# Kernel tuning notes

Hardware: AMD Instinct MI355X
Metric: run time of the kernel (lower is better)

## Reference

```python
import jax, jax.numpy as jnp
import numpy as np

NUM_BINS = 10
HIST_RANGE = 10.0
LN_EPS = 1e-5
NUM_SERVERS = 64
START_IDX = 2 + 2 + NUM_SERVERS  # = 68


def layer_norm(x, g, b):
    mu = jnp.mean(x, axis=-1, keepdims=True)
    var = jnp.mean(jnp.square(x - mu), axis=-1, keepdims=True)
    return (x - mu) * jax.lax.rsqrt(var + LN_EPS) * g + b


def batched_histogram(w):
    # w: [B, S]; replicates np.histogram(w_i, bins=10, range=(0,10)) per row,
    # then normalizes by (sum + 1e-8). Values outside [0,10] are excluded;
    # value == 10 falls in the last bin.
    idx = jnp.clip(jnp.floor(w * (NUM_BINS / HIST_RANGE)).astype(jnp.int32), 0, NUM_BINS - 1)
    mask = ((w >= 0.0) & (w <= HIST_RANGE)).astype(w.dtype)
    oh = jax.nn.one_hot(idx, NUM_BINS, dtype=w.dtype) * mask[..., None]  # [B,S,NB]
    hist = jnp.sum(oh, axis=1)  # [B,NB]
    return hist / (jnp.sum(hist, axis=-1, keepdims=True) + 1e-8)


def setup_inputs() -> dict:
    key = jax.random.key(0)
    ks = jax.random.split(key, 16)
    B, OBS, ACT, H, NB = 65536, 512, 64, 128, NUM_BINS
    COMB = (OBS - NUM_SERVERS) + 128 + 64  # 640

    def lin(k, fin, fout):
        bound = 1.0 / np.sqrt(fin)
        kw, kb = jax.random.split(k)
        return (jax.random.uniform(kw, (fin, fout), jnp.float32, -bound, bound),
                jax.random.uniform(kb, (fout,), jnp.float32, -bound, bound))

    obs = jax.random.uniform(ks[0], (B, OBS), jnp.float32, 0.0, 10.0)
    preference = jax.random.uniform(ks[1], (B, 2), jnp.float32)
    h_w1, h_b1 = lin(ks[2], NB, H)
    h_w2, h_b2 = lin(ks[3], H, H)
    p_w, p_b = lin(ks[4], 2, 64)
    s_w1, s_b1 = lin(ks[5], COMB, 256)
    s_w2, s_b2 = lin(ks[6], 256, 256)
    qd_w, qd_b = lin(ks[7], 256, ACT)
    qe_w, qe_b = lin(ks[8], 256, ACT)
    return {
        'obs': obs, 'preference': preference,
        'h_w1': h_w1, 'h_b1': h_b1,
        'h_ln1_g': jnp.ones((H,)), 'h_ln1_b': jnp.zeros((H,)),
        'h_w2': h_w2, 'h_b2': h_b2,
        'h_ln2_g': jnp.ones((H,)), 'h_ln2_b': jnp.zeros((H,)),
        'p_w': p_w, 'p_b': p_b,
        'p_ln_g': jnp.ones((64,)), 'p_ln_b': jnp.zeros((64,)),
        's_w1': s_w1, 's_b1': s_b1,
        's_ln1_g': jnp.ones((256,)), 's_ln1_b': jnp.zeros((256,)),
        's_w2': s_w2, 's_b2': s_b2,
        's_ln2_g': jnp.ones((256,)), 's_ln2_b': jnp.zeros((256,)),
        'qd_w': qd_w, 'qd_b': qd_b, 'qe_w': qe_w, 'qe_b': qe_b,
    }


def reference(obs, preference,
              h_w1, h_b1, h_ln1_g, h_ln1_b, h_w2, h_b2, h_ln2_g, h_ln2_b,
              p_w, p_b, p_ln_g, p_ln_b,
              s_w1, s_b1, s_ln1_g, s_ln1_b, s_w2, s_b2, s_ln2_g, s_ln2_b,
              qd_w, qd_b, qe_w, qe_b):
    server_workloads = obs[:, START_IDX:START_IDX + NUM_SERVERS]
    obs_wo = jnp.concatenate([obs[:, :START_IDX], obs[:, START_IDX + NUM_SERVERS:]], axis=-1)

    hist = batched_histogram(server_workloads)  # [B, 10]
    h = layer_norm(jax.nn.relu(hist @ h_w1 + h_b1), h_ln1_g, h_ln1_b)
    h = layer_norm(jax.nn.relu(h @ h_w2 + h_b2), h_ln2_g, h_ln2_b)  # [B,128]

    p = layer_norm(jax.nn.relu(preference @ p_w + p_b), p_ln_g, p_ln_b)  # [B,64]

    combined = jnp.concatenate([obs_wo, h, p], axis=-1)  # [B,640]
    s = layer_norm(jax.nn.relu(combined @ s_w1 + s_b1), s_ln1_g, s_ln1_b)
    s = layer_norm(jax.nn.relu(s @ s_w2 + s_b2), s_ln2_g, s_ln2_b)  # [B,256]

    q_delay = s @ qd_w + qd_b   # [B,A]
    q_energy = s @ qe_w + qe_b  # [B,A]
    return jnp.stack([q_delay, q_energy], axis=-1)  # [B,A,2]
```

## Files before the change

kernel.cpp:

```cpp
#include <hip/hip_runtime.h>

typedef __bf16 bf16x8 __attribute__((ext_vector_type(8)));
typedef __bf16 bf16x4 __attribute__((ext_vector_type(4)));
typedef float  f32x4  __attribute__((ext_vector_type(4)));

#define OFF_W1  0
#define OFF_W2  163840
#define OFF_WQ  229376
#define OFF_WH1 262144
#define OFF_WH2 266240
#define WS_ELEMS 282624

__global__ __launch_bounds__(256) void prep_kernel(
    const float* __restrict__ s_w1, const float* __restrict__ s_w2,
    const float* __restrict__ qd_w, const float* __restrict__ qe_w,
    const float* __restrict__ h_w1, const float* __restrict__ h_w2,
    __bf16* __restrict__ wsb)
{
  int idx = blockIdx.x * 256 + threadIdx.x;
  if (idx >= WS_ELEMS) return;
  float val = 0.f;
  if (idx < OFF_W2) {
    int t = idx;
    int j = t & 7, l = (t >> 3) & 63, rest = t >> 9;
    int nt = rest & 15, ks = rest >> 4;
    int k = ks * 32 + (l >> 4) * 8 + j, n = nt * 16 + (l & 15);
    val = s_w1[k * 256 + n];
  } else if (idx < OFF_WQ) {
    int t = idx - OFF_W2;
    int j = t & 7, l = (t >> 3) & 63, rest = t >> 9;
    int nt = rest & 15, ks = rest >> 4;
    int k = ks * 32 + (l >> 4) * 8 + j, n = nt * 16 + (l & 15);
    val = s_w2[k * 256 + n];
  } else if (idx < OFF_WH1) {
    int t = idx - OFF_WQ;
    int j = t & 7, l = (t >> 3) & 63, rest = t >> 9;
    int nt = rest & 7, ks = rest >> 3;
    int k = ks * 32 + (l >> 4) * 8 + j, n = nt * 16 + (l & 15);
    int a = n >> 1;
    val = (n & 1) ? qe_w[k * 64 + a] : qd_w[k * 64 + a];
  } else if (idx < OFF_WH2) {
    int t = idx - OFF_WH1;
    int j = t & 7, l = (t >> 3) & 63, rest = t >> 9;
    int nt = rest & 7;
    int k = (l >> 4) * 8 + j, n = nt * 16 + (l & 15);
    val = (k < 10) ? h_w1[k * 128 + n] : 0.f;
  } else {
    int t = idx - OFF_WH2;
    int j = t & 7, l = (t >> 3) & 63, rest = t >> 9;
    int nt = rest & 7, ks = rest >> 3;
    int k = ks * 32 + (l >> 4) * 8 + j, n = nt * 16 + (l & 15);
    val = h_w2[k * 128 + n];
  }
  wsb[idx] = (__bf16)val;
}

template<int KSTEPS, int NT_TOT, int NTW>
__device__ __forceinline__ void run_gemm(const __bf16* A, int astride,
    const bf16x8* __restrict__ Bsw, int wave, int lane, f32x4 acc[2][NTW])
{
  const int quad = lane >> 4, ln = lane & 15;
  const int ntb = wave * NTW;
  constexpr int PF = (KSTEPS >= 2) ? 2 : 1;
  bf16x8 bbuf[PF][NTW];
#pragma unroll
  for (int p = 0; p < PF; ++p)
#pragma unroll
    for (int i = 0; i < NTW; ++i)
      bbuf[p][i] = Bsw[(p * NT_TOT + ntb + i) * 64 + lane];
#pragma unroll
  for (int ks = 0; ks < KSTEPS; ++ks) {
    bf16x8 a[2];
#pragma unroll
    for (int mt = 0; mt < 2; ++mt)
      a[mt] = *(const bf16x8*)(A + (mt * 16 + ln) * astride + ks * 32 + quad * 8);
    bf16x8 bcur[NTW];
#pragma unroll
    for (int i = 0; i < NTW; ++i) bcur[i] = bbuf[ks % PF][i];
    if (ks + PF < KSTEPS) {
#pragma unroll
      for (int i = 0; i < NTW; ++i)
        bbuf[ks % PF][i] = Bsw[((ks + PF) * NT_TOT + ntb + i) * 64 + lane];
    }
#pragma unroll
    for (int mt = 0; mt < 2; ++mt)
#pragma unroll
      for (int i = 0; i < NTW; ++i)
        acc[mt][i] = __builtin_amdgcn_mfma_f32_16x16x32_bf16(a[mt], bcur[i], acc[mt][i], 0, 0, 0);
  }
}

template<int W, int NTW>
__device__ __forceinline__ void epilogue_ln(f32x4 acc[2][NTW],
    const float* __restrict__ bias, const float* __restrict__ g, const float* __restrict__ bb,
    __bf16* Adst, int dstride, int dstcol0,
    float* red_s, float* red_q, int wave, int lane)
{
  const int quad = lane >> 4, ln = lane & 15;
  float bv[NTW];
#pragma unroll
  for (int i = 0; i < NTW; ++i) bv[i] = bias[(wave * NTW + i) * 16 + ln];
#pragma unroll
  for (int mt = 0; mt < 2; ++mt) {
    float s[4] = {0, 0, 0, 0}, q[4] = {0, 0, 0, 0};
#pragma unroll
    for (int i = 0; i < NTW; ++i)
#pragma unroll
      for (int r = 0; r < 4; ++r) {
        float x = fmaxf(acc[mt][i][r] + bv[i], 0.f);
        s[r] += x; q[r] += x * x;
      }
#pragma unroll
    for (int m2 = 1; m2 < 16; m2 <<= 1)
#pragma unroll
      for (int r = 0; r < 4; ++r) {
        s[r] += __shfl_xor(s[r], m2, 64);
        q[r] += __shfl_xor(q[r], m2, 64);
      }
    if (ln == 0) {
#pragma unroll
      for (int r = 0; r < 4; ++r) {
        int m = mt * 16 + quad * 4 + r;
        red_s[wave * 32 + m] = s[r];
        red_q[wave * 32 + m] = q[r];
      }
    }
  }
  __syncthreads();
#pragma unroll
  for (int mt = 0; mt < 2; ++mt)
#pragma unroll
    for (int r = 0; r < 4; ++r) {
      int m = mt * 16 + quad * 4 + r;
      float tot = 0.f, totq = 0.f;
#pragma unroll
      for (int w2 = 0; w2 < 8; ++w2) { tot += red_s[w2 * 32 + m]; totq += red_q[w2 * 32 + m]; }
      float mu = tot / (float)W;
      float var = totq / (float)W - mu * mu;
      float rs = rsqrtf(var + 1e-5f);
#pragma unroll
      for (int i = 0; i < NTW; ++i) {
        int n = (wave * NTW + i) * 16 + ln;
        float x = fmaxf(acc[mt][i][r] + bv[i], 0.f);
        float o = (x - mu) * rs * g[n] + bb[n];
        Adst[m * dstride + dstcol0 + n] = (__bf16)o;
      }
    }
  __syncthreads();
}

__global__ __launch_bounds__(512)
__attribute__((amdgpu_waves_per_eu(4, 4)))
void critic_kernel(
    const float* __restrict__ obs, const float* __restrict__ pref,
    const float* __restrict__ h_b1, const float* __restrict__ h_g1, const float* __restrict__ h_bb1,
    const float* __restrict__ h_b2, const float* __restrict__ h_g2, const float* __restrict__ h_bb2,
    const float* __restrict__ p_w, const float* __restrict__ p_b,
    const float* __restrict__ p_g, const float* __restrict__ p_bb,
    const float* __restrict__ s_b1, const float* __restrict__ s_g1, const float* __restrict__ s_bb1,
    const float* __restrict__ s_b2, const float* __restrict__ s_g2, const float* __restrict__ s_bb2,
    const float* __restrict__ qd_b, const float* __restrict__ qe_b,
    const __bf16* __restrict__ wsb, float* __restrict__ out)
{
  __shared__ __align__(16) __bf16 A_comb[32 * 648];
  __shared__ __align__(16) __bf16 A_s[32 * 264];
  __shared__ __align__(16) __bf16 A_h[32 * 40];
  __shared__ float red_s[256];
  __shared__ float red_q[256];

  const int tid = threadIdx.x;
  const int wave = tid >> 6, lane = tid & 63;
  const int rowbase = blockIdx.x * 32;

  float pw0 = p_w[lane], pw1 = p_w[64 + lane], pb = p_b[lane];
  float pg = p_g[lane], pbb = p_bb[lane];
#pragma unroll
  for (int r = 0; r < 4; ++r) {
    int row = wave * 4 + r;
    int grow = rowbase + row;
    const float* orow = obs + (size_t)grow * 512;
    {
      int col = lane * 4;
      int src = (col < 68) ? col : col + 64;
      float4 v = *(const float4*)(orow + src);
      bf16x4 b4 = { (__bf16)v.x, (__bf16)v.y, (__bf16)v.z, (__bf16)v.w };
      *(bf16x4*)&A_comb[row * 648 + col] = b4;
    }
    if (lane < 48) {
      int col = 256 + lane * 4;
      float4 v = *(const float4*)(orow + col + 64);
      bf16x4 b4 = { (__bf16)v.x, (__bf16)v.y, (__bf16)v.z, (__bf16)v.w };
      *(bf16x4*)&A_comb[row * 648 + col] = b4;
    }
    float w = orow[68 + lane];
    int bi = (int)floorf(w);
    bi = bi < 0 ? 0 : (bi > 9 ? 9 : bi);
    bool valid = (w >= 0.f) && (w <= 10.f);
    float tot = 0.f, mine = 0.f;
#pragma unroll
    for (int b = 0; b < 10; ++b) {
      unsigned long long mk = __ballot(valid && (bi == b));
      float c = (float)__popcll(mk);
      tot += c;
      if (lane == b) mine = c;
    }
    float inv = 1.f / (tot + 1e-8f);
    if (lane < 32) A_h[row * 40 + lane] = (__bf16)((lane < 10) ? mine * inv : 0.f);
    float a0 = pref[grow * 2], a1 = pref[grow * 2 + 1];
    float v = fmaxf(fmaf(a0, pw0, fmaf(a1, pw1, pb)), 0.f);
    float s1 = v, s2 = v * v;
#pragma unroll
    for (int m2 = 1; m2 < 64; m2 <<= 1) {
      s1 += __shfl_xor(s1, m2, 64);
      s2 += __shfl_xor(s2, m2, 64);
    }
    float mu = s1 * (1.f / 64.f);
    float var = s2 * (1.f / 64.f) - mu * mu;
    float o = (v - mu) * rsqrtf(var + 1e-5f) * pg + pbb;
    A_comb[row * 648 + 576 + lane] = (__bf16)o;
  }
  __syncthreads();

  {
    f32x4 acc[2][1] = {};
    run_gemm<1, 8, 1>(A_h, 40, (const bf16x8*)(wsb + OFF_WH1), wave, lane, acc);
    epilogue_ln<128, 1>(acc, h_b1, h_g1, h_bb1, A_s, 264, 0, red_s, red_q, wave, lane);
  }
  {
    f32x4 acc[2][1] = {};
    run_gemm<4, 8, 1>(A_s, 264, (const bf16x8*)(wsb + OFF_WH2), wave, lane, acc);
    epilogue_ln<128, 1>(acc, h_b2, h_g2, h_bb2, A_comb, 648, 448, red_s, red_q, wave, lane);
  }
  {
    f32x4 acc[2][2] = {};
    run_gemm<20, 16, 2>(A_comb, 648, (const bf16x8*)(wsb + OFF_W1), wave, lane, acc);
    epilogue_ln<256, 2>(acc, s_b1, s_g1, s_bb1, A_s, 264, 0, red_s, red_q, wave, lane);
  }
  {
    f32x4 acc[2][2] = {};
    run_gemm<8, 16, 2>(A_s, 264, (const bf16x8*)(wsb + OFF_W2), wave, lane, acc);
    epilogue_ln<256, 2>(acc, s_b2, s_g2, s_bb2, A_s, 264, 0, red_s, red_q, wave, lane);
  }
  {
    f32x4 acc[2][1] = {};
    run_gemm<8, 8, 1>(A_s, 264, (const bf16x8*)(wsb + OFF_WQ), wave, lane, acc);
    const int quad = lane >> 4, ln = lane & 15;
    int n = wave * 16 + ln;
    float qb = (n & 1) ? qe_b[n >> 1] : qd_b[n >> 1];
#pragma unroll
    for (int mt = 0; mt < 2; ++mt)
#pragma unroll
      for (int r = 0; r < 4; ++r) {
        int m = mt * 16 + quad * 4 + r;
        out[(size_t)(rowbase + m) * 128 + n] = acc[mt][0][r] + qb;
      }
  }
}

extern "C" void kernel_launch(void* const* d_in, const int* in_sizes, int n_in,
                              void* d_out, int out_size, void* d_ws, size_t ws_size,
                              hipStream_t stream) {
  const float* obs    = (const float*)d_in[0];
  const float* pref   = (const float*)d_in[1];
  const float* h_w1   = (const float*)d_in[2];
  const float* h_b1   = (const float*)d_in[3];
  const float* h_g1   = (const float*)d_in[4];
  const float* h_bb1  = (const float*)d_in[5];
  const float* h_w2   = (const float*)d_in[6];
  const float* h_b2   = (const float*)d_in[7];
  const float* h_g2   = (const float*)d_in[8];
  const float* h_bb2  = (const float*)d_in[9];
  const float* p_w    = (const float*)d_in[10];
  const float* p_b    = (const float*)d_in[11];
  const float* p_g    = (const float*)d_in[12];
  const float* p_bb   = (const float*)d_in[13];
  const float* s_w1   = (const float*)d_in[14];
  const float* s_b1   = (const float*)d_in[15];
  const float* s_g1   = (const float*)d_in[16];
  const float* s_bb1  = (const float*)d_in[17];
  const float* s_w2   = (const float*)d_in[18];
  const float* s_b2   = (const float*)d_in[19];
  const float* s_g2   = (const float*)d_in[20];
  const float* s_bb2  = (const float*)d_in[21];
  const float* qd_w   = (const float*)d_in[22];
  const float* qd_b   = (const float*)d_in[23];
  const float* qe_w   = (const float*)d_in[24];
  const float* qe_b   = (const float*)d_in[25];

  __bf16* wsb = (__bf16*)d_ws;
  int B = in_sizes[0] / 512;
  int nblocks = B / 32;

  prep_kernel<<<(WS_ELEMS + 255) / 256, 256, 0, stream>>>(s_w1, s_w2, qd_w, qe_w, h_w1, h_w2, wsb);
  critic_kernel<<<nblocks, 512, 0, stream>>>(
      obs, pref, h_b1, h_g1, h_bb1, h_b2, h_g2, h_bb2,
      p_w, p_b, p_g, p_bb, s_b1, s_g1, s_bb1, s_b2, s_g2, s_bb2,
      qd_b, qe_b, (const __bf16*)wsb, (float*)d_out);
}
```

Before: 404.6 us.

## Split fused critic kernel into frontend and s-MLP kernels via bf16 global buffer

```diff
diff --git a/kernel.cpp b/kernel.cpp
--- a/kernel.cpp
+++ b/kernel.cpp
@@ -10,6 +10,7 @@
 #define OFF_WH1 262144
 #define OFF_WH2 266240
 #define WS_ELEMS 282624
+#define OFF_COMB 282624
 
 __global__ __launch_bounds__(256) void prep_kernel(
     const float* __restrict__ s_w1, const float* __restrict__ s_w2,
@@ -55,45 +56,43 @@
   wsb[idx] = (__bf16)val;
 }
 
-template<int KSTEPS, int NT_TOT, int NTW>
+template<int MT, int KSTEPS, int NT_TOT, int NTW>
 __device__ __forceinline__ void run_gemm(const __bf16* A, int astride,
-    const bf16x8* __restrict__ Bsw, int wave, int lane, f32x4 acc[2][NTW])
+    const bf16x8* __restrict__ Bsw, int wave, int lane, f32x4 acc[MT][NTW])
 {
   const int quad = lane >> 4, ln = lane & 15;
   const int ntb = wave * NTW;
-  constexpr int PF = (KSTEPS >= 2) ? 2 : 1;
-  bf16x8 bbuf[PF][NTW];
-#pragma unroll
-  for (int p = 0; p < PF; ++p)
-#pragma unroll
-    for (int i = 0; i < NTW; ++i)
-      bbuf[p][i] = Bsw[(p * NT_TOT + ntb + i) * 64 + lane];
+  bf16x8 bcur[NTW];
+#pragma unroll
+  for (int i = 0; i < NTW; ++i) bcur[i] = Bsw[(ntb + i) * 64 + lane];
 #pragma unroll
   for (int ks = 0; ks < KSTEPS; ++ks) {
-    bf16x8 a[2];
-#pragma unroll
-    for (int mt = 0; mt < 2; ++mt)
+    bf16x8 bnxt[NTW];
+    if (ks + 1 < KSTEPS) {
+#pragma unroll
+      for (int i = 0; i < NTW; ++i)
+        bnxt[i] = Bsw[((ks + 1) * NT_TOT + ntb + i) * 64 + lane];
+    }
+    bf16x8 a[MT];
+#pragma unroll
+    for (int mt = 0; mt < MT; ++mt)
       a[mt] = *(const bf16x8*)(A + (mt * 16 + ln) * astride + ks * 32 + quad * 8);
-    bf16x8 bcur[NTW];
-#pragma unroll
-    for (int i = 0; i < NTW; ++i) bcur[i] = bbuf[ks % PF][i];
-    if (ks + PF < KSTEPS) {
-#pragma unroll
-      for (int i = 0; i < NTW; ++i)
-        bbuf[ks % PF][i] = Bsw[((ks + PF) * NT_TOT + ntb + i) * 64 + lane];
-    }
-#pragma unroll
-    for (int mt = 0; mt < 2; ++mt)
+#pragma unroll
+    for (int mt = 0; mt < MT; ++mt)
 #pragma unroll
       for (int i = 0; i < NTW; ++i)
         acc[mt][i] = __builtin_amdgcn_mfma_f32_16x16x32_bf16(a[mt], bcur[i], acc[mt][i], 0, 0, 0);
-  }
-}
-
-template<int W, int NTW>
-__device__ __forceinline__ void epilogue_ln(f32x4 acc[2][NTW],
+    if (ks + 1 < KSTEPS) {
+#pragma unroll
+      for (int i = 0; i < NTW; ++i) bcur[i] = bnxt[i];
+    }
+  }
+}
+
+template<int MT, int W, int NTW, int NWAVES>
+__device__ __forceinline__ void epilogue_ln(f32x4 acc[MT][NTW],
     const float* __restrict__ bias, const float* __restrict__ g, const float* __restrict__ bb,
-    __bf16* Adst, int dstride, int dstcol0,
+    __bf16* dst, int dstride, int dstcol0,
     float* red_s, float* red_q, int wave, int lane)
 {
   const int quad = lane >> 4, ln = lane & 15;
@@ -101,7 +100,7 @@
 #pragma unroll
   for (int i = 0; i < NTW; ++i) bv[i] = bias[(wave * NTW + i) * 16 + ln];
 #pragma unroll
-  for (int mt = 0; mt < 2; ++mt) {
+  for (int mt = 0; mt < MT; ++mt) {
     float s[4] = {0, 0, 0, 0}, q[4] = {0, 0, 0, 0};
 #pragma unroll
     for (int i = 0; i < NTW; ++i)
@@ -121,20 +120,20 @@
 #pragma unroll
       for (int r = 0; r < 4; ++r) {
         int m = mt * 16 + quad * 4 + r;
-        red_s[wave * 32 + m] = s[r];
-        red_q[wave * 32 + m] = q[r];
+        red_s[wave * (MT * 16) + m] = s[r];
+        red_q[wave * (MT * 16) + m] = q[r];
       }
     }
   }
   __syncthreads();
 #pragma unroll
-  for (int mt = 0; mt < 2; ++mt)
+  for (int mt = 0; mt < MT; ++mt)
 #pragma unroll
     for (int r = 0; r < 4; ++r) {
       int m = mt * 16 + quad * 4 + r;
       float tot = 0.f, totq = 0.f;
 #pragma unroll
-      for (int w2 = 0; w2 < 8; ++w2) { tot += red_s[w2 * 32 + m]; totq += red_q[w2 * 32 + m]; }
+      for (int w2 = 0; w2 < NWAVES; ++w2) { tot += red_s[w2 * (MT * 16) + m]; totq += red_q[w2 * (MT * 16) + m]; }
       float mu = tot / (float)W;
       float var = totq / (float)W - mu * mu;
       float rs = rsqrtf(var + 1e-5f);
@@ -143,54 +142,49 @@
         int n = (wave * NTW + i) * 16 + ln;
         float x = fmaxf(acc[mt][i][r] + bv[i], 0.f);
         float o = (x - mu) * rs * g[n] + bb[n];
-        Adst[m * dstride + dstcol0 + n] = (__bf16)o;
+        dst[m * dstride + dstcol0 + n] = (__bf16)o;
       }
     }
   __syncthreads();
 }
 
-__global__ __launch_bounds__(512)
-__attribute__((amdgpu_waves_per_eu(4, 4)))
-void critic_kernel(
+__global__ __launch_bounds__(256) void frontend_kernel(
     const float* __restrict__ obs, const float* __restrict__ pref,
     const float* __restrict__ h_b1, const float* __restrict__ h_g1, const float* __restrict__ h_bb1,
     const float* __restrict__ h_b2, const float* __restrict__ h_g2, const float* __restrict__ h_bb2,
     const float* __restrict__ p_w, const float* __restrict__ p_b,
     const float* __restrict__ p_g, const float* __restrict__ p_bb,
-    const float* __restrict__ s_b1, const float* __restrict__ s_g1, const float* __restrict__ s_bb1,
-    const float* __restrict__ s_b2, const float* __restrict__ s_g2, const float* __restrict__ s_bb2,
-    const float* __restrict__ qd_b, const float* __restrict__ qe_b,
-    const __bf16* __restrict__ wsb, float* __restrict__ out)
-{
-  __shared__ __align__(16) __bf16 A_comb[32 * 648];
-  __shared__ __align__(16) __bf16 A_s[32 * 264];
-  __shared__ __align__(16) __bf16 A_h[32 * 40];
+    const __bf16* __restrict__ wsb, __bf16* __restrict__ comb)
+{
+  __shared__ __align__(16) __bf16 A_h[64 * 40];
+  __shared__ __align__(16) __bf16 A_s[64 * 136];
   __shared__ float red_s[256];
   __shared__ float red_q[256];
 
   const int tid = threadIdx.x;
   const int wave = tid >> 6, lane = tid & 63;
-  const int rowbase = blockIdx.x * 32;
+  const int rowbase = blockIdx.x * 64;
 
   float pw0 = p_w[lane], pw1 = p_w[64 + lane], pb = p_b[lane];
   float pg = p_g[lane], pbb = p_bb[lane];
-#pragma unroll
-  for (int r = 0; r < 4; ++r) {
-    int row = wave * 4 + r;
+#pragma unroll 1
+  for (int r = 0; r < 16; ++r) {
+    int row = wave * 16 + r;
     int grow = rowbase + row;
     const float* orow = obs + (size_t)grow * 512;
+    __bf16* crow = comb + (size_t)grow * 640;
     {
       int col = lane * 4;
       int src = (col < 68) ? col : col + 64;
       float4 v = *(const float4*)(orow + src);
       bf16x4 b4 = { (__bf16)v.x, (__bf16)v.y, (__bf16)v.z, (__bf16)v.w };
-      *(bf16x4*)&A_comb[row * 648 + col] = b4;
+      *(bf16x4*)(crow + col) = b4;
     }
     if (lane < 48) {
       int col = 256 + lane * 4;
       float4 v = *(const float4*)(orow + col + 64);
       bf16x4 b4 = { (__bf16)v.x, (__bf16)v.y, (__bf16)v.z, (__bf16)v.w };
-      *(bf16x4*)&A_comb[row * 648 + col] = b4;
+      *(bf16x4*)(crow + col) = b4;
     }
     float w = orow[68 + lane];
     int bi = (int)floorf(w);
@@ -217,33 +211,66 @@
     float mu = s1 * (1.f / 64.f);
     float var = s2 * (1.f / 64.f) - mu * mu;
     float o = (v - mu) * rsqrtf(var + 1e-5f) * pg + pbb;
-    A_comb[row * 648 + 576 + lane] = (__bf16)o;
+    crow[576 + lane] = (__bf16)o;
   }
   __syncthreads();
 
   {
+    f32x4 acc[4][2] = {};
+    run_gemm<4, 1, 8, 2>(A_h, 40, (const bf16x8*)(wsb + OFF_WH1), wave, lane, acc);
+    epilogue_ln<4, 128, 2, 4>(acc, h_b1, h_g1, h_bb1, A_s, 136, 0, red_s, red_q, wave, lane);
+  }
+  {
+    f32x4 acc[4][2] = {};
+    run_gemm<4, 4, 8, 2>(A_s, 136, (const bf16x8*)(wsb + OFF_WH2), wave, lane, acc);
+    epilogue_ln<4, 128, 2, 4>(acc, h_b2, h_g2, h_bb2,
+                              comb + (size_t)rowbase * 640, 640, 448, red_s, red_q, wave, lane);
+  }
+}
+
+__global__ __launch_bounds__(512) void smlp_kernel(
+    const float* __restrict__ s_b1, const float* __restrict__ s_g1, const float* __restrict__ s_bb1,
+    const float* __restrict__ s_b2, const float* __restrict__ s_g2, const float* __restrict__ s_bb2,
+    const float* __restrict__ qd_b, const float* __restrict__ qe_b,
+    const __bf16* __restrict__ wsb, const __bf16* __restrict__ comb,
+    float* __restrict__ out)
+{
+  __shared__ __align__(16) __bf16 A_comb[32 * 648];
+  __shared__ __align__(16) __bf16 A_s[32 * 264];
+  __shared__ float red_s[256];
+  __shared__ float red_q[256];
+
+  const int tid = threadIdx.x;
+  const int wave = tid >> 6, lane = tid & 63;
+  const int rowbase = blockIdx.x * 32;
+
+  {
+    const __bf16* src = comb + (size_t)(rowbase + wave * 4) * 640;
+    __bf16* dstb = A_comb + wave * 4 * 648;
+#pragma unroll
+    for (int it = 0; it < 5; ++it) {
+      int local = it * 64 + lane;
+      int rl = local / 80;
+      int ch = local - rl * 80;
+      bf16x8 v = *(const bf16x8*)(src + rl * 640 + ch * 8);
+      *(bf16x8*)(dstb + rl * 648 + ch * 8) = v;
+    }
+  }
+  __syncthreads();
+
+  {
+    f32x4 acc[2][2] = {};
+    run_gemm<2, 20, 16, 2>(A_comb, 648, (const bf16x8*)(wsb + OFF_W1), wave, lane, acc);
+    epilogue_ln<2, 256, 2, 8>(acc, s_b1, s_g1, s_bb1, A_s, 264, 0, red_s, red_q, wave, lane);
+  }
+  {
+    f32x4 acc[2][2] = {};
+    run_gemm<2, 8, 16, 2>(A_s, 264, (const bf16x8*)(wsb + OFF_W2), wave, lane, acc);
+    epilogue_ln<2, 256, 2, 8>(acc, s_b2, s_g2, s_bb2, A_s, 264, 0, red_s, red_q, wave, lane);
+  }
+  {
     f32x4 acc[2][1] = {};
-    run_gemm<1, 8, 1>(A_h, 40, (const bf16x8*)(wsb + OFF_WH1), wave, lane, acc);
-    epilogue_ln<128, 1>(acc, h_b1, h_g1, h_bb1, A_s, 264, 0, red_s, red_q, wave, lane);
-  }
-  {
-    f32x4 acc[2][1] = {};
-    run_gemm<4, 8, 1>(A_s, 264, (const bf16x8*)(wsb + OFF_WH2), wave, lane, acc);
-    epilogue_ln<128, 1>(acc, h_b2, h_g2, h_bb2, A_comb, 648, 448, red_s, red_q, wave, lane);
-  }
-  {
-    f32x4 acc[2][2] = {};
-    run_gemm<20, 16, 2>(A_comb, 648, (const bf16x8*)(wsb + OFF_W1), wave, lane, acc);
-    epilogue_ln<256, 2>(acc, s_b1, s_g1, s_bb1, A_s, 264, 0, red_s, red_q, wave, lane);
-  }
-  {
-    f32x4 acc[2][2] = {};
-    run_gemm<8, 16, 2>(A_s, 264, (const bf16x8*)(wsb + OFF_W2), wave, lane, acc);
-    epilogue_ln<256, 2>(acc, s_b2, s_g2, s_bb2, A_s, 264, 0, red_s, red_q, wave, lane);
-  }
-  {
-    f32x4 acc[2][1] = {};
-    run_gemm<8, 8, 1>(A_s, 264, (const bf16x8*)(wsb + OFF_WQ), wave, lane, acc);
+    run_gemm<2, 8, 8, 1>(A_s, 264, (const bf16x8*)(wsb + OFF_WQ), wave, lane, acc);
     const int quad = lane >> 4, ln = lane & 15;
     int n = wave * 16 + ln;
     float qb = (n & 1) ? qe_b[n >> 1] : qd_b[n >> 1];
@@ -288,12 +315,14 @@
   const float* qe_b   = (const float*)d_in[25];
 
   __bf16* wsb = (__bf16*)d_ws;
+  __bf16* comb = wsb + OFF_COMB;
   int B = in_sizes[0] / 512;
-  int nblocks = B / 32;
 
   prep_kernel<<<(WS_ELEMS + 255) / 256, 256, 0, stream>>>(s_w1, s_w2, qd_w, qe_w, h_w1, h_w2, wsb);
-  critic_kernel<<<nblocks, 512, 0, stream>>>(
+  frontend_kernel<<<B / 64, 256, 0, stream>>>(
       obs, pref, h_b1, h_g1, h_bb1, h_b2, h_g2, h_bb2,
-      p_w, p_b, p_g, p_bb, s_b1, s_g1, s_bb1, s_b2, s_g2, s_bb2,
-      qd_b, qe_b, (const __bf16*)wsb, (float*)d_out);
-}
+      p_w, p_b, p_g, p_bb, (const __bf16*)wsb, comb);
+  smlp_kernel<<<B / 32, 512, 0, stream>>>(
+      s_b1, s_g1, s_bb1, s_b2, s_g2, s_bb2,
+      qd_b, qe_b, (const __bf16*)wsb, (const __bf16*)comb, (float*)d_out);
+}
```

New measurement: 441.8 us. +9.2%, slower.
